# Optimization experiments

Hardware: AMD Instinct MI355X
Metric: run time of the kernel (lower is better)

The kernel has to match this reference:

```python
import jax, jax.numpy as jnp
import numpy as np

N = 50000          # nodes
E_RAND = 590000    # random edges (+ N self-loops -> E = 640000)
IN_F = 128
OUT_F = 128
H, D = 8, 16       # num_heads, head_dim (H*D == OUT_F)
HOP = 5
ALPHA = 0.1
SLOPE = 0.2
EPS = 1e-5


def _layer_norm(x, g, b):
    mu = jnp.mean(x, axis=-1, keepdims=True)
    var = jnp.mean((x - mu) ** 2, axis=-1, keepdims=True)
    return (x - mu) * jax.lax.rsqrt(var + EPS) * g + b


def setup_inputs() -> dict:
    key = jax.random.key(0)
    ks = jax.random.split(key, 10)
    loops = jnp.arange(N, dtype=jnp.int32)  # self-loops -> no 0-in-degree nodes
    src = jnp.concatenate([loops, jax.random.randint(ks[0], (E_RAND,), 0, N, dtype=jnp.int32)])
    dst = jnp.concatenate([loops, jax.random.randint(ks[1], (E_RAND,), 0, N, dtype=jnp.int32)])
    s = 0.05  # xavier-like small init gain
    return {
        "feat": jax.random.normal(ks[2], (N, IN_F), jnp.float32),
        "src": src,
        "dst": dst,
        "w_head": jax.random.normal(ks[3], (OUT_F, IN_F), jnp.float32) * s,
        "w_tail": jax.random.normal(ks[4], (OUT_F, IN_F), jnp.float32) * s,
        "w_ent": jax.random.normal(ks[5], (OUT_F, IN_F), jnp.float32) * s,
        "attn": jax.random.normal(ks[6], (1, H, D), jnp.float32) * s,
        "ln1_g": jnp.ones((IN_F,), jnp.float32),
        "ln1_b": jnp.zeros((IN_F,), jnp.float32),
        "ln2_g": jnp.ones((OUT_F,), jnp.float32),
        "ln2_b": jnp.zeros((OUT_F,), jnp.float32),
        "ff_w1": jax.random.normal(ks[7], (4 * OUT_F, OUT_F), jnp.float32) * s,
        "ff_b1": jnp.zeros((4 * OUT_F,), jnp.float32),
        "ff_w2": jax.random.normal(ks[8], (OUT_F, 4 * OUT_F), jnp.float32) * s,
        "ff_b2": jnp.zeros((OUT_F,), jnp.float32),
    }


def _forward(src, dst, feat, w_head, w_tail, w_ent, attn,
             ln1_g, ln1_b, ln2_g, ln2_b, ff_w1, ff_b1, ff_w2, ff_b2):
    ones = jnp.ones(src.shape[0], jnp.float32)
    out_deg = jnp.clip(jax.ops.segment_sum(ones, src, num_segments=N), 1.0)  # [N]
    in_deg = jnp.clip(jax.ops.segment_sum(ones, dst, num_segments=N), 1.0)
    head_norm = out_deg ** -0.5
    tail_norm = in_deg ** 0.5
    log_in = jnp.log1p(in_deg)  # graph.dstdata['log_in'] (log of in-degree, set at graph build time)

    x = _layer_norm(feat, ln1_g, ln1_b)  # graph_layer_norm (feat_drop=0 in eval)
    fh = (x @ w_head.T).reshape(N, H, D) * head_norm[:, None, None]
    ft = (x @ w_tail.T).reshape(N, H, D) * head_norm[:, None, None]
    fe = (x @ w_ent.T).reshape(N, H, D) * head_norm[:, None, None]

    # edge attention logits: u_mul_v -> leaky_relu -> dot with attn vector
    lr = jax.nn.leaky_relu(fh[src] * ft[dst], SLOPE)  # [E,H,D]
    e = jnp.einsum('ehd,xhd->eh', lr, attn)           # [E,H]
    e = e * log_in[dst][:, None] / D                  # e_mul_v with log_in, / head_dim

    # edge softmax grouped by destination node, per head
    seg_max = jax.ops.segment_max(e, dst, num_segments=N)
    e_exp = jnp.exp(e - seg_max[dst])
    denom = jax.ops.segment_sum(e_exp, dst, num_segments=N)
    a = e_exp / denom[dst]                            # [E,H]

    # PPR diffusion (ppr_estimation), attn_drop=0 in eval
    feat0 = fe
    h = feat0
    for hop in range(HOP):
        if hop > 0:
            h = h * head_norm[:, None, None]
        m = h[src] * a[:, :, None]                    # [E,H,D] u_mul_e
        h = jax.ops.segment_sum(m, dst, num_segments=N)  # fn.sum
        h = h * tail_norm[:, None, None]
        h = (1.0 - ALPHA) * h + ALPHA * feat0

    rst = h + feat.reshape(N, H, D)  # res_fc is Identity since in_feats == out_feats
    rst = rst.reshape(N, OUT_F)
    ff = _layer_norm(rst, ln2_g, ln2_b)
    ff = jax.nn.relu(ff @ ff_w1.T + ff_b1) @ ff_w2.T + ff_b2  # PositionWiseFeedForward
    return ff + rst


def reference(feat, src, dst, w_head, w_tail, w_ent, attn, ln1_g, ln1_b,
              ln2_g, ln2_b, ff_w1, ff_b1, ff_w2, ff_b2):
    return _forward(src, dst, feat, w_head, w_tail, w_ent, attn,
                    ln1_g, ln1_b, ln2_g, ln2_b, ff_w1, ff_b1, ff_w2, ff_b2)
```

## Files before the change

kernel.cpp:

```cpp
#include <hip/hip_runtime.h>
#include <hip/hip_bf16.h>

typedef __attribute__((ext_vector_type(8))) short bf16x8;
typedef __attribute__((ext_vector_type(4))) float f32x4;
typedef unsigned int uint32;

#define F 128
#define HOPS 5
#define LDS_STRIDE 68
#define W1_STRIDE 136
#define W2_STRIDE 72
#define TB_STRIDE 72

__device__ __forceinline__ float b2f(__hip_bfloat16 h) { return __bfloat162float(h); }
__device__ __forceinline__ __hip_bfloat16 f2b(float f) { return __float2bfloat16(f); }

__device__ __forceinline__ float load_in(const void* p, size_t i, int isbf) {
    return isbf ? __bfloat162float(((const __hip_bfloat16*)p)[i]) : ((const float*)p)[i];
}

__device__ __forceinline__ float bflo(uint32 u) { union { uint32 i; float f; } v; v.i = u << 16; return v.f; }
__device__ __forceinline__ float bfhi(uint32 u) { union { uint32 i; float f; } v; v.i = u & 0xffff0000u; return v.f; }
__device__ __forceinline__ uint32 packbf2(float a, float b) {
    __hip_bfloat16 ha = f2b(a), hb = f2b(b);
    unsigned short ua = *(unsigned short*)&ha, ub = *(unsigned short*)&hb;
    return ((uint32)ub << 16) | ua;
}

__device__ __forceinline__ float edge_dot(uint4 gv, const float* ftf, const float* at) {
    float acc = 0.f;
    uint32 us[4] = {gv.x, gv.y, gv.z, gv.w};
    #pragma unroll
    for (int k = 0; k < 4; ++k) {
        float f0 = bflo(us[k]) * ftf[2 * k];
        float f1 = bfhi(us[k]) * ftf[2 * k + 1];
        f0 = fmaxf(f0, 0.2f * f0);
        f1 = fmaxf(f1, 0.2f * f1);
        acc = fmaf(f0, at[2 * k], acc);
        acc = fmaf(f1, at[2 * k + 1], acc);
    }
    return acc;
}

__global__ void detect_k(const uint32* __restrict__ w, int* flag) {
    __shared__ int cnt[256];
    int t = threadIdx.x;
    uint32 x = w[t * 97];
    int e_low = (x >> 7) & 0xFF;
    cnt[t] = (e_low >= 110 && e_low <= 135) ? 1 : 0;
    __syncthreads();
    for (int s = 128; s > 0; s >>= 1) {
        if (t < s) cnt[t] += cnt[t + s];
        __syncthreads();
    }
    if (t == 0) flag[0] = (cnt[0] >= 160) ? 1 : 0;
}

__global__ void cvt_all_k(const void* __restrict__ w_head, const void* __restrict__ w_tail,
                          const void* __restrict__ w_ent, const void* __restrict__ ff_w1,
                          const void* __restrict__ ff_w2, const void* __restrict__ attn,
                          const void* __restrict__ ff_b1, const void* __restrict__ ff_b2,
                          const int* __restrict__ flag,
                          __hip_bfloat16* __restrict__ wblob, float* __restrict__ fblob) {
    int i = blockIdx.x * blockDim.x + threadIdx.x;
    int isbf = flag[0];
    if (i < 180224) {
        const void* srcp; int j;
        if (i < 16384)       { srcp = w_head; j = i; }
        else if (i < 32768)  { srcp = w_tail; j = i - 16384; }
        else if (i < 49152)  { srcp = w_ent;  j = i - 32768; }
        else if (i < 114688) { srcp = ff_w1;  j = i - 49152; }
        else                 { srcp = ff_w2;  j = i - 114688; }
        wblob[i] = f2b(load_in(srcp, j, isbf));
    } else if (i < 180992) {
        int k = i - 180224;
        const void* srcp; int j;
        if (k < 128)      { srcp = attn;  j = k; }
        else if (k < 640) { srcp = ff_b1; j = k - 128; }
        else              { srcp = ff_b2; j = k - 640; }
        fblob[k] = load_in(srcp, j, isbf);
    }
}

__global__ void degree_k(const int* __restrict__ src, const int* __restrict__ dst,
                         int* in8, int* out8, int E, int N) {
    int i = blockIdx.x * blockDim.x + threadIdx.x;
    int slice = blockIdx.x & 7;
    if (i < E) {
        atomicAdd(&in8[slice * N + dst[i]], 1);
        atomicAdd(&out8[slice * N + src[i]], 1);
    }
}

__global__ void scan1_k(const int* __restrict__ in8, int* partial, int* blk_sum, int N) {
    __shared__ int sh[256];
    int t = threadIdx.x;
    int i = blockIdx.x * 256 + t;
    int c = 0;
    if (i < N) {
#pragma unroll
        for (int s = 0; s < 8; ++s) c += in8[s * N + i];
    }
    sh[t] = c;
    __syncthreads();
    for (int o = 1; o < 256; o <<= 1) {
        int v = (t >= o) ? sh[t - o] : 0;
        __syncthreads();
        sh[t] += v;
        __syncthreads();
    }
    if (i < N) partial[i] = sh[t] - c;
    if (t == 255) blk_sum[blockIdx.x] = sh[255];
}

__global__ void scan2_k(const int* __restrict__ blk_sum, int* blk_off, int nb,
                        int* row_ptr, int N) {
    __shared__ int sh[256];
    int t = threadIdx.x;
    if (nb <= 256) {
        int v = (t < nb) ? blk_sum[t] : 0;
        sh[t] = v;
        __syncthreads();
        for (int o = 1; o < 256; o <<= 1) {
            int u = (t >= o) ? sh[t - o] : 0;
            __syncthreads();
            sh[t] += u;
            __syncthreads();
        }
        if (t < nb) blk_off[t] = sh[t] - v;
        if (t == 255) row_ptr[N] = sh[255];
    } else if (t == 0) {
        int run = 0;
        for (int b = 0; b < nb; ++b) { blk_off[b] = run; run += blk_sum[b]; }
        row_ptr[N] = run;
    }
}

__global__ void scan3_norms_k(const int* __restrict__ partial, const int* __restrict__ blk_off,
                              const int* __restrict__ in8, const int* __restrict__ out8,
                              int* row_ptr, int* soff, float* head_norm, float* tail_norm,
                              float* log_in, int N) {
    int i = blockIdx.x * 256 + threadIdx.x;
    if (i >= N) return;
    row_ptr[i] = partial[i] + blk_off[blockIdx.x];
    int run = 0;
#pragma unroll
    for (int s = 0; s < 8; ++s) { soff[s * N + i] = run; run += in8[s * N + i]; }
    int od = 0;
#pragma unroll
    for (int s = 0; s < 8; ++s) od += out8[s * N + i];
    float id = fmaxf((float)run, 1.0f);
    float odf = fmaxf((float)od, 1.0f);
    head_norm[i] = rsqrtf(odf);
    tail_norm[i] = sqrtf(id);
    log_in[i] = log1pf(id);
}

__global__ void scatter_k(const int* __restrict__ src, const int* __restrict__ dst,
                          const int* __restrict__ row_ptr, const int* __restrict__ soff,
                          int* cursor8, int* csr_src, int E, int N) {
    int i = blockIdx.x * blockDim.x + threadIdx.x;
    int slice = blockIdx.x & 7;
    if (i < E) {
        int d = dst[i];
        int p = row_ptr[d] + soff[slice * N + d] + atomicAdd(&cursor8[slice * N + d], 1);
        csr_src[p] = src[i];
    }
}

__global__ void ln1_k(const void* __restrict__ x, const void* __restrict__ g,
                      const void* __restrict__ b, const int* __restrict__ flag,
                      __hip_bfloat16* __restrict__ y, int N) {
    int w = blockIdx.x * (blockDim.x >> 6) + (threadIdx.x >> 6);
    if (w >= N) return;
    int isbf = flag[0];
    int t = threadIdx.x & 63;
    float v0 = load_in(x, (size_t)w * F + t, isbf);
    float v1 = load_in(x, (size_t)w * F + t + 64, isbf);
    float s = v0 + v1, sq = v0 * v0 + v1 * v1;
    for (int m = 1; m < 64; m <<= 1) { s += __shfl_xor(s, m, 64); sq += __shfl_xor(sq, m, 64); }
    float mu = s * (1.0f / F);
    float var = fmaxf(sq * (1.0f / F) - mu * mu, 0.0f);
    float r = rsqrtf(var + 1e-5f);
    y[(size_t)w * F + t]      = f2b((v0 - mu) * r * load_in(g, t, isbf) + load_in(b, t, isbf));
    y[(size_t)w * F + t + 64] = f2b((v1 - mu) * r * load_in(g, t + 64, isbf) + load_in(b, t + 64, isbf));
}

__global__ void ln2_k(const float* __restrict__ x, const void* __restrict__ g,
                      const void* __restrict__ b, const int* __restrict__ flag,
                      __hip_bfloat16* __restrict__ y, int N) {
    int w = blockIdx.x * (blockDim.x >> 6) + (threadIdx.x >> 6);
    if (w >= N) return;
    int isbf = flag[0];
    int t = threadIdx.x & 63;
    float v0 = x[(size_t)w * F + t], v1 = x[(size_t)w * F + t + 64];
    float s = v0 + v1, sq = v0 * v0 + v1 * v1;
    for (int m = 1; m < 64; m <<= 1) { s += __shfl_xor(s, m, 64); sq += __shfl_xor(sq, m, 64); }
    float mu = s * (1.0f / F);
    float var = fmaxf(sq * (1.0f / F) - mu * mu, 0.0f);
    float r = rsqrtf(var + 1e-5f);
    y[(size_t)w * F + t]      = f2b((v0 - mu) * r * load_in(g, t, isbf) + load_in(b, t, isbf));
    y[(size_t)w * F + t + 64] = f2b((v1 - mu) * r * load_in(g, t + 64, isbf) + load_in(b, t + 64, isbf));
}

__global__ void proj_gemm_k(const __hip_bfloat16* __restrict__ X,
                            const __hip_bfloat16* __restrict__ Wall,
                            const float* __restrict__ head_norm,
                            __hip_bfloat16* __restrict__ fh,
                            __hip_bfloat16* __restrict__ ft,
                            uint32* __restrict__ fe_bf, int N) {
    __shared__ __align__(16) char smem[2 * 64 * W1_STRIDE * 2];
    __hip_bfloat16* lx = (__hip_bfloat16*)smem;
    __hip_bfloat16* lw = (__hip_bfloat16*)(smem + 64 * W1_STRIDE * 2);
    float* eps = (float*)smem;
    int tid = threadIdx.x;
    int wv = tid >> 6, lane = tid & 63;
    int lr = lane & 15, quad = lane >> 4;
    int bm = blockIdx.x * 64;
    int g = blockIdx.y;
    int wsel = g >> 1;
    int wcb = (g & 1) * 64;
    {
        const __hip_bfloat16* xs = X + (size_t)bm * F;
        size_t maxe = (size_t)N * F;
#pragma unroll
        for (int i = 0; i < 4; ++i) {
            int idx = i * 2048 + tid * 8;
            int n = idx >> 7, k = idx & 127;
            size_t gi = (size_t)bm * F + idx;
            uint4 v = (gi + 8 <= maxe) ? *(const uint4*)(xs + idx)
                                       : *(const uint4*)(X + maxe - 8);
            *(uint4*)&lx[n * W1_STRIDE + k] = v;
        }
        const __hip_bfloat16* ws = Wall + ((size_t)wsel * F + wcb) * F;
#pragma unroll
        for (int i = 0; i < 4; ++i) {
            int idx = i * 2048 + tid * 8;
            int n = idx >> 7, k = idx & 127;
            *(uint4*)&lw[n * W1_STRIDE + k] = *(const uint4*)(ws + idx);
        }
    }
    __syncthreads();
    f32x4 acc[4] = {{0,0,0,0},{0,0,0,0},{0,0,0,0},{0,0,0,0}};
#pragma unroll
    for (int ks = 0; ks < 4; ++ks) {
        bf16x8 a = *reinterpret_cast<const bf16x8*>(&lx[(wv * 16 + lr) * W1_STRIDE + ks * 32 + quad * 8]);
#pragma unroll
        for (int j = 0; j < 4; ++j) {
            bf16x8 bb = *reinterpret_cast<const bf16x8*>(&lw[(j * 16 + lr) * W1_STRIDE + ks * 32 + quad * 8]);
            acc[j] = __builtin_amdgcn_mfma_f32_16x16x32_bf16(a, bb, acc[j], 0, 0, 0);
        }
    }
    __syncthreads();
    int rl = wv * 16 + quad * 4;
#pragma unroll
    for (int j = 0; j < 4; ++j)
#pragma unroll
        for (int r = 0; r < 4; ++r)
            eps[(rl + r) * LDS_STRIDE + j * 16 + lr] = acc[j][r];
    __syncthreads();
    int tr = tid >> 4, tc = (tid & 15) * 4;
#pragma unroll
    for (int p = 0; p < 4; ++p) {
        int row_l = p * 16 + tr;
        int grow = bm + row_l;
        if (grow >= N) continue;
        float4 v = *(const float4*)&eps[row_l * LDS_STRIDE + tc];
        float hn = head_norm[grow];
        v.x *= hn; v.y *= hn; v.z *= hn; v.w *= hn;
        size_t idx = (size_t)grow * F + wcb + tc;
        uint2 u; u.x = packbf2(v.x, v.y); u.y = packbf2(v.z, v.w);
        __hip_bfloat16* dstp = (wsel == 0) ? fh : (wsel == 1) ? ft : (__hip_bfloat16*)fe_bf;
        *(uint2*)&dstp[idx] = u;
    }
}

__global__ void attn_soft_k(const int* __restrict__ csr_src, const int* __restrict__ row_ptr,
                            const uint32* __restrict__ fh2, const uint32* __restrict__ ft2,
                            const float* __restrict__ attn_f, const float* __restrict__ log_in,
                            float* __restrict__ e_buf, float* __restrict__ inv_arr, int N) {
    int w = blockIdx.x * (blockDim.x >> 6) + (threadIdx.x >> 6);
    if (w >= N) return;
    int t = threadIdx.x & 63;
    int g = t >> 4, j = t & 15;
    int b = row_ptr[w], e = row_ptr[w + 1];
    uint4 fr = ((const uint4*)ft2)[(size_t)w * 16 + j];
    float ftf[8] = {bflo(fr.x), bfhi(fr.x), bflo(fr.y), bfhi(fr.y),
                    bflo(fr.z), bfhi(fr.z), bflo(fr.w), bfhi(fr.w)};
    float at[8];
#pragma unroll
    for (int k = 0; k < 8; ++k) at[k] = attn_f[8 * j + k];
    float scale = log_in[w] * (1.0f / 16.0f);
    float m = -1e30f;
    for (int p0 = b; p0 < e; p0 += 8) {
        int pa = p0 + g, pb = p0 + 4 + g;
        bool oka = pa < e, okb = pb < e;
        int sa = csr_src[oka ? pa : b];
        int sb = csr_src[okb ? pb : b];
        uint4 ga = ((const uint4*)fh2)[(size_t)sa * 16 + j];
        uint4 gb = ((const uint4*)fh2)[(size_t)sb * 16 + j];
        float ra = edge_dot(ga, ftf, at);
        float rb = edge_dot(gb, ftf, at);
        ra += __shfl_xor(ra, 1, 64);
        rb += __shfl_xor(rb, 1, 64);
        float la = ra * scale, lb = rb * scale;
        if (oka) { if (!(j & 1)) e_buf[(size_t)pa * 8 + (j >> 1)] = la; m = fmaxf(m, la); }
        if (okb) { if (!(j & 1)) e_buf[(size_t)pb * 8 + (j >> 1)] = lb; m = fmaxf(m, lb); }
    }
    m = fmaxf(m, __shfl_xor(m, 16, 64));
    m = fmaxf(m, __shfl_xor(m, 32, 64));
    float mh = __shfl(m, (t & 7) * 2, 64);
    float sum = 0.f;
    for (size_t base = (size_t)b * 8 + t; base < (size_t)e * 8; base += 64) {
        float ex = expf(e_buf[base] - mh);
        e_buf[base] = ex;
        sum += ex;
    }
    sum += __shfl_xor(sum, 8, 64);
    sum += __shfl_xor(sum, 16, 64);
    sum += __shfl_xor(sum, 32, 64);
    float inv = 1.0f / fmaxf(sum, 1e-30f);
    if (t < 8) inv_arr[(size_t)w * 8 + t] = inv;
}

__global__ void hop_k(const uint32* __restrict__ gsrc2, const float* __restrict__ e_exp,
                      const float* __restrict__ inv_arr,
                      const int* __restrict__ csr_src, const int* __restrict__ row_ptr,
                      const float* __restrict__ tail_norm, const float* __restrict__ head_norm,
                      const uint32* __restrict__ fe_bf, const void* __restrict__ feat,
                      const int* __restrict__ flag,
                      uint32* __restrict__ out_bf, float* __restrict__ out_f32,
                      int last, int N) {
    int w = blockIdx.x * 8 + (threadIdx.x >> 5);
    if (w >= N) return;
    int l = threadIdx.x & 31;
    int h = l >> 2;
    int b = row_ptr[w], e = row_ptr[w + 1];
    float inv = inv_arr[(size_t)w * 8 + h];
    float a0 = 0.f, a1 = 0.f, a2 = 0.f, a3 = 0.f;
    int p = b;
    for (; p + 8 <= e; p += 8) {
        int s[8]; float av[8]; uint2 gg[8];
#pragma unroll
        for (int i = 0; i < 8; ++i) s[i] = csr_src[p + i];
#pragma unroll
        for (int i = 0; i < 8; ++i) av[i] = e_exp[(size_t)(p + i) * 8 + h];
#pragma unroll
        for (int i = 0; i < 8; ++i) gg[i] = ((const uint2*)gsrc2)[(size_t)s[i] * 32 + l];
#pragma unroll
        for (int i = 0; i < 8; ++i) {
            a0 += bflo(gg[i].x) * av[i]; a1 += bfhi(gg[i].x) * av[i];
            a2 += bflo(gg[i].y) * av[i]; a3 += bfhi(gg[i].y) * av[i];
        }
    }
    if (p < e) {
        int s[8]; float av[8]; uint2 gg[8];
#pragma unroll
        for (int i = 0; i < 8; ++i) {
            int q = p + i;
            bool ok = q < e;
            int q2 = ok ? q : b;
            s[i] = csr_src[q2];
            av[i] = ok ? e_exp[(size_t)q * 8 + h] : 0.f;
        }
#pragma unroll
        for (int i = 0; i < 8; ++i) gg[i] = ((const uint2*)gsrc2)[(size_t)s[i] * 32 + l];
#pragma unroll
        for (int i = 0; i < 8; ++i) {
            a0 += bflo(gg[i].x) * av[i]; a1 += bfhi(gg[i].x) * av[i];
            a2 += bflo(gg[i].y) * av[i]; a3 += bfhi(gg[i].y) * av[i];
        }
    }
    float tl = tail_norm[w] * 0.9f * inv;
    uint2 feu = ((const uint2*)fe_bf)[(size_t)w * 32 + l];
    float r0 = tl * a0 + 0.1f * bflo(feu.x);
    float r1 = tl * a1 + 0.1f * bfhi(feu.x);
    float r2 = tl * a2 + 0.1f * bflo(feu.y);
    float r3 = tl * a3 + 0.1f * bfhi(feu.y);
    if (last) {
        int isbf = flag[0];
        float4 o;
        if (isbf) {
            uint2 fu = ((const uint2*)feat)[(size_t)w * 32 + l];
            o.x = r0 + bflo(fu.x); o.y = r1 + bfhi(fu.x);
            o.z = r2 + bflo(fu.y); o.w = r3 + bfhi(fu.y);
        } else {
            float4 fv = ((const float4*)feat)[(size_t)w * 32 + l];
            o.x = r0 + fv.x; o.y = r1 + fv.y; o.z = r2 + fv.z; o.w = r3 + fv.w;
        }
        ((float4*)out_f32)[(size_t)w * 32 + l] = o;
    } else {
        float hn = head_norm[w];
        uint2 u;
        u.x = packbf2(r0 * hn, r1 * hn);
        u.y = packbf2(r2 * hn, r3 * hn);
        ((uint2*)out_bf)[(size_t)w * 32 + l] = u;
    }
}

__global__ __launch_bounds__(256, 2)
void ffn_fused_k(const __hip_bfloat16* __restrict__ Y, const __hip_bfloat16* __restrict__ W1,
                 const __hip_bfloat16* __restrict__ W2, const float* __restrict__ b1f,
                 const float* __restrict__ b2f, const float* __restrict__ rst,
                 const int* __restrict__ flag, void* __restrict__ out, int N) {
    __shared__ __align__(16) char smem[45056];
    __hip_bfloat16* lw1 = (__hip_bfloat16*)smem;
    __hip_bfloat16* lw2 = (__hip_bfloat16*)(smem + 17408);
    __hip_bfloat16* tb  = (__hip_bfloat16*)(smem + 35840);
    float* eps = (float*)smem;
    int tid = threadIdx.x;
    int wv = tid >> 6, lane = tid & 63;
    int lr = lane & 15, quad = lane >> 4;
    int bm = blockIdx.x * 64;
    int row_a = bm + wv * 16 + lr;
    if (row_a >= N) row_a = N - 1;
    bf16x8 ay[4];
    {
        const __hip_bfloat16* yr = Y + (size_t)row_a * F + quad * 8;
#pragma unroll
        for (int ks = 0; ks < 4; ++ks) ay[ks] = *reinterpret_cast<const bf16x8*>(yr + ks * 32);
    }
    f32x4 o[8];
#pragma unroll
    for (int j = 0; j < 8; ++j) o[j] = (f32x4){0,0,0,0};
    __hip_bfloat16* tbuf = tb + wv * (16 * TB_STRIDE);
    for (int c = 0; c < 8; ++c) {
        int nb0 = c * 64;
        __syncthreads();
        {
            const __hip_bfloat16* s1 = W1 + (size_t)nb0 * F;
#pragma unroll
            for (int i = 0; i < 4; ++i) {
                int idx = i * 2048 + tid * 8;
                int n = idx >> 7, k = idx & 127;
                *(uint4*)&lw1[n * W1_STRIDE + k] = *(const uint4*)(s1 + idx);
            }
#pragma unroll
            for (int i = 0; i < 4; ++i) {
                int idx = i * 2048 + tid * 8;
                int r = idx >> 6, k2 = idx & 63;
                *(uint4*)&lw2[r * W2_STRIDE + k2] = *(const uint4*)(W2 + (size_t)r * 512 + nb0 + k2);
            }
        }
        __syncthreads();
        f32x4 t[4] = {{0,0,0,0},{0,0,0,0},{0,0,0,0},{0,0,0,0}};
#pragma unroll
        for (int ks = 0; ks < 4; ++ks) {
#pragma unroll
            for (int j = 0; j < 4; ++j) {
                bf16x8 bb = *reinterpret_cast<const bf16x8*>(&lw1[(j * 16 + lr) * W1_STRIDE + ks * 32 + quad * 8]);
                t[j] = __builtin_amdgcn_mfma_f32_16x16x32_bf16(ay[ks], bb, t[j], 0, 0, 0);
            }
        }
#pragma unroll
        for (int j = 0; j < 4; ++j) {
            float bias = b1f[nb0 + 16 * j + lr];
#pragma unroll
            for (int r = 0; r < 4; ++r) {
                float v = fmaxf(t[j][r] + bias, 0.f);
                tbuf[(quad * 4 + r) * TB_STRIDE + j * 16 + lr] = f2b(v);
            }
        }
#pragma unroll
        for (int ks2 = 0; ks2 < 2; ++ks2) {
            bf16x8 at = *reinterpret_cast<const bf16x8*>(&tbuf[lr * TB_STRIDE + ks2 * 32 + quad * 8]);
#pragma unroll
            for (int j2 = 0; j2 < 8; ++j2) {
                bf16x8 bb = *reinterpret_cast<const bf16x8*>(&lw2[(j2 * 16 + lr) * W2_STRIDE + ks2 * 32 + quad * 8]);
                o[j2] = __builtin_amdgcn_mfma_f32_16x16x32_bf16(at, bb, o[j2], 0, 0, 0);
            }
        }
    }
    __syncthreads();
    int rl = wv * 16 + quad * 4;
#pragma unroll
    for (int j = 0; j < 8; ++j)
#pragma unroll
        for (int r = 0; r < 4; ++r)
            eps[(rl + r) * 132 + j * 16 + lr] = o[j][r];
    __syncthreads();
    int isbf = flag[0];
#pragma unroll
    for (int p = 0; p < 8; ++p) {
        int idx = p * 1024 + tid * 4;
        int row_l = idx >> 7, col = idx & 127;
        int grow = bm + row_l;
        if (grow >= N) continue;
        float4 v = *(const float4*)&eps[row_l * 132 + col];
        float4 bias = *(const float4*)&b2f[col];
        float4 rv = *(const float4*)&rst[(size_t)grow * F + col];
        v.x += bias.x + rv.x; v.y += bias.y + rv.y;
        v.z += bias.z + rv.z; v.w += bias.w + rv.w;
        size_t gidx = (size_t)grow * F + col;
        if (isbf) {
            uint2 u; u.x = packbf2(v.x, v.y); u.y = packbf2(v.z, v.w);
            *(uint2*)&((__hip_bfloat16*)out)[gidx] = u;
        } else {
            *(float4*)&((float*)out)[gidx] = v;
        }
    }
}

extern "C" void kernel_launch(void* const* d_in, const int* in_sizes, int n_in,
                              void* d_out, int out_size, void* d_ws, size_t ws_size,
                              hipStream_t stream) {
    if (n_in < 15) return;
    const void* feat = d_in[0];
    const int* src = (const int*)d_in[1];
    const int* dst = (const int*)d_in[2];
    const void* w_head = d_in[3];
    const void* w_tail = d_in[4];
    const void* w_ent  = d_in[5];
    const void* attn   = d_in[6];
    const void* ln1_g  = d_in[7];
    const void* ln1_b  = d_in[8];
    const void* ln2_g  = d_in[9];
    const void* ln2_b  = d_in[10];
    const void* ff_w1  = d_in[11];
    const void* ff_b1  = d_in[12];
    const void* ff_w2  = d_in[13];
    const void* ff_b2  = d_in[14];

    const int N = in_sizes[0] / F;
    const int E = in_sizes[1];
    (void)out_size;

    char* base = (char*)d_ws;
    size_t off = 0;
    auto alloc = [&](size_t bytes) -> void* {
        void* r = base + off;
        off += (bytes + 255) & ~(size_t)255;
        return r;
    };
    int* zr        = (int*)alloc((size_t)24 * N * 4);
    int* in8 = zr, * out8 = zr + 8 * N, * cursor8 = zr + 16 * N;
    int* soff      = (int*)alloc((size_t)8 * N * 4);
    int* row_ptr   = (int*)alloc((size_t)(N + 1) * 4);
    int* partial   = (int*)alloc((size_t)N * 4);
    int* blk_sum   = (int*)alloc((size_t)1024 * 4);
    int* blk_off   = (int*)alloc((size_t)1024 * 4);
    int* flag      = (int*)alloc(256);
    float* head_norm = (float*)alloc((size_t)N * 4);
    float* tail_norm = (float*)alloc((size_t)N * 4);
    float* log_in    = (float*)alloc((size_t)N * 4);
    float* inv_arr   = (float*)alloc((size_t)N * 8 * 4);
    int* csr_src   = (int*)alloc((size_t)E * 4);
    __hip_bfloat16* wh_bf = (__hip_bfloat16*)alloc((size_t)F * F * 2);
    __hip_bfloat16* wt_bf = (__hip_bfloat16*)alloc((size_t)F * F * 2);
    __hip_bfloat16* we_bf = (__hip_bfloat16*)alloc((size_t)F * F * 2);
    __hip_bfloat16* w1_bf = (__hip_bfloat16*)alloc((size_t)512 * F * 2);
    __hip_bfloat16* w2_bf = (__hip_bfloat16*)alloc((size_t)F * 512 * 2);
    float* attn_f    = (float*)alloc((size_t)F * 4);
    float* b1f       = (float*)alloc((size_t)512 * 4);
    float* b2f_      = (float*)alloc((size_t)F * 4);
    __hip_bfloat16* x_bf = (__hip_bfloat16*)alloc((size_t)N * F * 2);
    __hip_bfloat16* fh   = (__hip_bfloat16*)alloc((size_t)N * F * 2);
    __hip_bfloat16* ftb  = (__hip_bfloat16*)alloc((size_t)N * F * 2);
    float* e_a = (float*)alloc((size_t)E * 8 * 4);
    uint32* fe_bf = (uint32*)alloc((size_t)N * F * 2);
    uint32* hA_bf = (uint32*)alloc((size_t)N * F * 2);
    uint32* hB_bf = (uint32*)alloc((size_t)N * F * 2);
    float* rst = (float*)alloc((size_t)N * F * 4);
    __hip_bfloat16* y_bf = (__hip_bfloat16*)hA_bf;
    (void)wt_bf; (void)we_bf;
    if (off > ws_size) return;

    const int Mb = (N + 63) / 64;
    const int nodeBlocks = (N + 3) / 4;
    const int hopBlocks = (N + 7) / 8;
    const int nb = (N + 255) / 256;

    detect_k<<<1, 256, 0, stream>>>((const uint32*)feat, flag);
    cvt_all_k<<<(180992 + 255) / 256, 256, 0, stream>>>(w_head, w_tail, w_ent, ff_w1, ff_w2,
                                                        attn, ff_b1, ff_b2, flag, wh_bf, attn_f);

    hipMemsetAsync(zr, 0, (size_t)24 * N * 4, stream);
    degree_k<<<(E + 255) / 256, 256, 0, stream>>>(src, dst, in8, out8, E, N);
    scan1_k<<<nb, 256, 0, stream>>>(in8, partial, blk_sum, N);
    scan2_k<<<1, 256, 0, stream>>>(blk_sum, blk_off, nb, row_ptr, N);
    scan3_norms_k<<<nb, 256, 0, stream>>>(partial, blk_off, in8, out8,
                                          row_ptr, soff, head_norm, tail_norm, log_in, N);
    scatter_k<<<(E + 255) / 256, 256, 0, stream>>>(src, dst, row_ptr, soff, cursor8, csr_src, E, N);

    ln1_k<<<nodeBlocks, 256, 0, stream>>>(feat, ln1_g, ln1_b, flag, x_bf, N);
    proj_gemm_k<<<dim3(Mb, 6), 256, 0, stream>>>(x_bf, wh_bf, head_norm, fh, ftb, fe_bf, N);

    attn_soft_k<<<nodeBlocks, 256, 0, stream>>>(csr_src, row_ptr, (const uint32*)fh,
                                                (const uint32*)ftb, attn_f, log_in,
                                                e_a, inv_arr, N);

    const uint32* gsrc = fe_bf;
    uint32* bufs[2] = {hA_bf, hB_bf};
    for (int hop = 0; hop < HOPS; ++hop) {
        int last = (hop == HOPS - 1);
        uint32* dst_bf = last ? nullptr : bufs[hop & 1];
        hop_k<<<hopBlocks, 256, 0, stream>>>(gsrc, e_a, inv_arr, csr_src, row_ptr, tail_norm,
                                             head_norm, fe_bf, feat, flag, dst_bf, rst, last, N);
        if (!last) gsrc = dst_bf;
    }

    ln2_k<<<nodeBlocks, 256, 0, stream>>>(rst, ln2_g, ln2_b, flag, y_bf, N);
    ffn_fused_k<<<Mb, 256, 0, stream>>>(y_bf, w1_bf, w2_bf, b1f, b2f_, rst, flag, d_out, N);
}
```

Before: 468.5 us.

## Store attention weights in fp16, fuse LN2 into last hop, merge scan kernels

```diff
diff --git a/kernel.cpp b/kernel.cpp
--- a/kernel.cpp
+++ b/kernel.cpp
@@ -1,5 +1,6 @@
 #include <hip/hip_runtime.h>
 #include <hip/hip_bf16.h>
+#include <hip/hip_fp16.h>
 
 typedef __attribute__((ext_vector_type(8))) short bf16x8;
 typedef __attribute__((ext_vector_type(4))) float f32x4;
@@ -27,19 +28,18 @@
     return ((uint32)ub << 16) | ua;
 }
 
-__device__ __forceinline__ float edge_dot(uint4 gv, const float* ftf, const float* at) {
-    float acc = 0.f;
+__device__ __forceinline__ float edge_dot2(uint4 gv, const float* c1, const float* c2) {
+    float acc = 0.f, acc2 = 0.f;
     uint32 us[4] = {gv.x, gv.y, gv.z, gv.w};
     #pragma unroll
     for (int k = 0; k < 4; ++k) {
-        float f0 = bflo(us[k]) * ftf[2 * k];
-        float f1 = bfhi(us[k]) * ftf[2 * k + 1];
-        f0 = fmaxf(f0, 0.2f * f0);
-        f1 = fmaxf(f1, 0.2f * f1);
-        acc = fmaf(f0, at[2 * k], acc);
-        acc = fmaf(f1, at[2 * k + 1], acc);
-    }
-    return acc;
+        float f0 = bflo(us[k]), f1 = bfhi(us[k]);
+        acc  = fmaf(c1[2 * k],     f0,        acc);
+        acc2 = fmaf(c2[2 * k],     fabsf(f0), acc2);
+        acc  = fmaf(c1[2 * k + 1], f1,        acc);
+        acc2 = fmaf(c2[2 * k + 1], fabsf(f1), acc2);
+    }
+    return acc + acc2;
 }
 
 __global__ void detect_k(const uint32* __restrict__ w, int* flag) {
@@ -156,6 +156,38 @@
     log_in[i] = log1pf(id);
 }
 
+__global__ void scan3f_k(const int* __restrict__ partial, const int* __restrict__ blk_sum,
+                         int nb, const int* __restrict__ in8, const int* __restrict__ out8,
+                         int* row_ptr, int* soff, float* head_norm, float* tail_norm,
+                         float* log_in, int N) {
+    __shared__ int bs[256];
+    int t = threadIdx.x;
+    bs[t] = (t < nb) ? blk_sum[t] : 0;
+    __syncthreads();
+    for (int o = 1; o < 256; o <<= 1) {
+        int v = (t >= o) ? bs[t - o] : 0;
+        __syncthreads();
+        bs[t] += v;
+        __syncthreads();
+    }
+    if (blockIdx.x == 0 && t == 0) row_ptr[N] = bs[nb - 1];
+    int boff = (blockIdx.x == 0) ? 0 : bs[blockIdx.x - 1];
+    int i = blockIdx.x * 256 + t;
+    if (i >= N) return;
+    row_ptr[i] = partial[i] + boff;
+    int run = 0;
+#pragma unroll
+    for (int s = 0; s < 8; ++s) { soff[s * N + i] = run; run += in8[s * N + i]; }
+    int od = 0;
+#pragma unroll
+    for (int s = 0; s < 8; ++s) od += out8[s * N + i];
+    float id = fmaxf((float)run, 1.0f);
+    float odf = fmaxf((float)od, 1.0f);
+    head_norm[i] = rsqrtf(odf);
+    tail_norm[i] = sqrtf(id);
+    log_in[i] = log1pf(id);
+}
+
 __global__ void scatter_k(const int* __restrict__ src, const int* __restrict__ dst,
                           const int* __restrict__ row_ptr, const int* __restrict__ soff,
                           int* cursor8, int* csr_src, int E, int N) {
@@ -177,23 +209,6 @@
     int t = threadIdx.x & 63;
     float v0 = load_in(x, (size_t)w * F + t, isbf);
     float v1 = load_in(x, (size_t)w * F + t + 64, isbf);
-    float s = v0 + v1, sq = v0 * v0 + v1 * v1;
-    for (int m = 1; m < 64; m <<= 1) { s += __shfl_xor(s, m, 64); sq += __shfl_xor(sq, m, 64); }
-    float mu = s * (1.0f / F);
-    float var = fmaxf(sq * (1.0f / F) - mu * mu, 0.0f);
-    float r = rsqrtf(var + 1e-5f);
-    y[(size_t)w * F + t]      = f2b((v0 - mu) * r * load_in(g, t, isbf) + load_in(b, t, isbf));
-    y[(size_t)w * F + t + 64] = f2b((v1 - mu) * r * load_in(g, t + 64, isbf) + load_in(b, t + 64, isbf));
-}
-
-__global__ void ln2_k(const float* __restrict__ x, const void* __restrict__ g,
-                      const void* __restrict__ b, const int* __restrict__ flag,
-                      __hip_bfloat16* __restrict__ y, int N) {
-    int w = blockIdx.x * (blockDim.x >> 6) + (threadIdx.x >> 6);
-    if (w >= N) return;
-    int isbf = flag[0];
-    int t = threadIdx.x & 63;
-    float v0 = x[(size_t)w * F + t], v1 = x[(size_t)w * F + t + 64];
     float s = v0 + v1, sq = v0 * v0 + v1 * v1;
     for (int m = 1; m < 64; m <<= 1) { s += __shfl_xor(s, m, 64); sq += __shfl_xor(sq, m, 64); }
     float mu = s * (1.0f / F);
@@ -278,7 +293,8 @@
 __global__ void attn_soft_k(const int* __restrict__ csr_src, const int* __restrict__ row_ptr,
                             const uint32* __restrict__ fh2, const uint32* __restrict__ ft2,
                             const float* __restrict__ attn_f, const float* __restrict__ log_in,
-                            float* __restrict__ e_buf, float* __restrict__ inv_arr, int N) {
+                            float* __restrict__ e_buf, __half* __restrict__ e_h,
+                            float* __restrict__ inv_arr, int N) {
     int w = blockIdx.x * (blockDim.x >> 6) + (threadIdx.x >> 6);
     if (w >= N) return;
     int t = threadIdx.x & 63;
@@ -287,9 +303,13 @@
     uint4 fr = ((const uint4*)ft2)[(size_t)w * 16 + j];
     float ftf[8] = {bflo(fr.x), bfhi(fr.x), bflo(fr.y), bfhi(fr.y),
                     bflo(fr.z), bfhi(fr.z), bflo(fr.w), bfhi(fr.w)};
-    float at[8];
-#pragma unroll
-    for (int k = 0; k < 8; ++k) at[k] = attn_f[8 * j + k];
+    float c1[8], c2[8];
+#pragma unroll
+    for (int k = 0; k < 8; ++k) {
+        float at = attn_f[8 * j + k];
+        c1[k] = 0.6f * at * ftf[k];
+        c2[k] = 0.4f * at * fabsf(ftf[k]);
+    }
     float scale = log_in[w] * (1.0f / 16.0f);
     float m = -1e30f;
     for (int p0 = b; p0 < e; p0 += 8) {
@@ -299,8 +319,8 @@
         int sb = csr_src[okb ? pb : b];
         uint4 ga = ((const uint4*)fh2)[(size_t)sa * 16 + j];
         uint4 gb = ((const uint4*)fh2)[(size_t)sb * 16 + j];
-        float ra = edge_dot(ga, ftf, at);
-        float rb = edge_dot(gb, ftf, at);
+        float ra = edge_dot2(ga, c1, c2);
+        float rb = edge_dot2(gb, c1, c2);
         ra += __shfl_xor(ra, 1, 64);
         rb += __shfl_xor(rb, 1, 64);
         float la = ra * scale, lb = rb * scale;
@@ -313,7 +333,7 @@
     float sum = 0.f;
     for (size_t base = (size_t)b * 8 + t; base < (size_t)e * 8; base += 64) {
         float ex = expf(e_buf[base] - mh);
-        e_buf[base] = ex;
+        e_h[base] = __float2half(ex);
         sum += ex;
     }
     sum += __shfl_xor(sum, 8, 64);
@@ -323,11 +343,12 @@
     if (t < 8) inv_arr[(size_t)w * 8 + t] = inv;
 }
 
-__global__ void hop_k(const uint32* __restrict__ gsrc2, const float* __restrict__ e_exp,
+__global__ void hop_k(const uint32* __restrict__ gsrc2, const __half* __restrict__ e_h,
                       const float* __restrict__ inv_arr,
                       const int* __restrict__ csr_src, const int* __restrict__ row_ptr,
                       const float* __restrict__ tail_norm, const float* __restrict__ head_norm,
                       const uint32* __restrict__ fe_bf, const void* __restrict__ feat,
+                      const void* __restrict__ ln2g, const void* __restrict__ ln2b,
                       const int* __restrict__ flag,
                       uint32* __restrict__ out_bf, float* __restrict__ out_f32,
                       int last, int N) {
@@ -344,7 +365,7 @@
 #pragma unroll
         for (int i = 0; i < 8; ++i) s[i] = csr_src[p + i];
 #pragma unroll
-        for (int i = 0; i < 8; ++i) av[i] = e_exp[(size_t)(p + i) * 8 + h];
+        for (int i = 0; i < 8; ++i) av[i] = __half2float(e_h[(size_t)(p + i) * 8 + h]);
 #pragma unroll
         for (int i = 0; i < 8; ++i) gg[i] = ((const uint2*)gsrc2)[(size_t)s[i] * 32 + l];
 #pragma unroll
@@ -361,7 +382,7 @@
             bool ok = q < e;
             int q2 = ok ? q : b;
             s[i] = csr_src[q2];
-            av[i] = ok ? e_exp[(size_t)q * 8 + h] : 0.f;
+            av[i] = ok ? __half2float(e_h[(size_t)q * 8 + h]) : 0.f;
         }
 #pragma unroll
         for (int i = 0; i < 8; ++i) gg[i] = ((const uint2*)gsrc2)[(size_t)s[i] * 32 + l];
@@ -389,6 +410,24 @@
             o.x = r0 + fv.x; o.y = r1 + fv.y; o.z = r2 + fv.z; o.w = r3 + fv.w;
         }
         ((float4*)out_f32)[(size_t)w * 32 + l] = o;
+        float s2 = o.x + o.y + o.z + o.w;
+        float sq = o.x * o.x + o.y * o.y + o.z * o.z + o.w * o.w;
+#pragma unroll
+        for (int mm = 1; mm < 32; mm <<= 1) {
+            s2 += __shfl_xor(s2, mm, 64);
+            sq += __shfl_xor(sq, mm, 64);
+        }
+        float mu = s2 * (1.0f / F);
+        float var = fmaxf(sq * (1.0f / F) - mu * mu, 0.0f);
+        float rr = rsqrtf(var + 1e-5f);
+        float g0 = load_in(ln2g, 4 * l + 0, isbf), g1 = load_in(ln2g, 4 * l + 1, isbf);
+        float g2 = load_in(ln2g, 4 * l + 2, isbf), g3 = load_in(ln2g, 4 * l + 3, isbf);
+        float b0 = load_in(ln2b, 4 * l + 0, isbf), b1 = load_in(ln2b, 4 * l + 1, isbf);
+        float b2 = load_in(ln2b, 4 * l + 2, isbf), b3 = load_in(ln2b, 4 * l + 3, isbf);
+        uint2 u;
+        u.x = packbf2((o.x - mu) * rr * g0 + b0, (o.y - mu) * rr * g1 + b1);
+        u.y = packbf2((o.z - mu) * rr * g2 + b2, (o.w - mu) * rr * g3 + b3);
+        ((uint2*)out_bf)[(size_t)w * 32 + l] = u;
     } else {
         float hn = head_norm[w];
         uint2 u;
@@ -562,6 +601,7 @@
     uint32* hB_bf = (uint32*)alloc((size_t)N * F * 2);
     float* rst = (float*)alloc((size_t)N * F * 4);
     __hip_bfloat16* y_bf = (__hip_bfloat16*)hA_bf;
+    __half* e_h = (__half*)x_bf;
     (void)wt_bf; (void)we_bf;
     if (off > ws_size) return;
 
@@ -577,9 +617,14 @@
     hipMemsetAsync(zr, 0, (size_t)24 * N * 4, stream);
     degree_k<<<(E + 255) / 256, 256, 0, stream>>>(src, dst, in8, out8, E, N);
     scan1_k<<<nb, 256, 0, stream>>>(in8, partial, blk_sum, N);
-    scan2_k<<<1, 256, 0, stream>>>(blk_sum, blk_off, nb, row_ptr, N);
-    scan3_norms_k<<<nb, 256, 0, stream>>>(partial, blk_off, in8, out8,
-                                          row_ptr, soff, head_norm, tail_norm, log_in, N);
+    if (nb <= 256) {
+        scan3f_k<<<nb, 256, 0, stream>>>(partial, blk_sum, nb, in8, out8,
+                                         row_ptr, soff, head_norm, tail_norm, log_in, N);
+    } else {
+        scan2_k<<<1, 256, 0, stream>>>(blk_sum, blk_off, nb, row_ptr, N);
+        scan3_norms_k<<<nb, 256, 0, stream>>>(partial, blk_off, in8, out8,
+                                              row_ptr, soff, head_norm, tail_norm, log_in, N);
+    }
     scatter_k<<<(E + 255) / 256, 256, 0, stream>>>(src, dst, row_ptr, soff, cursor8, csr_src, E, N);
 
     ln1_k<<<nodeBlocks, 256, 0, stream>>>(feat, ln1_g, ln1_b, flag, x_bf, N);
@@ -587,18 +632,18 @@
 
     attn_soft_k<<<nodeBlocks, 256, 0, stream>>>(csr_src, row_ptr, (const uint32*)fh,
                                                 (const uint32*)ftb, attn_f, log_in,
-                                                e_a, inv_arr, N);
+                                                e_a, e_h, inv_arr, N);
 
     const uint32* gsrc = fe_bf;
     uint32* bufs[2] = {hA_bf, hB_bf};
     for (int hop = 0; hop < HOPS; ++hop) {
         int last = (hop == HOPS - 1);
-        uint32* dst_bf = last ? nullptr : bufs[hop & 1];
-        hop_k<<<hopBlocks, 256, 0, stream>>>(gsrc, e_a, inv_arr, csr_src, row_ptr, tail_norm,
-                                             head_norm, fe_bf, feat, flag, dst_bf, rst, last, N);
+        uint32* dst_bf = last ? (uint32*)y_bf : bufs[hop & 1];
+        hop_k<<<hopBlocks, 256, 0, stream>>>(gsrc, e_h, inv_arr, csr_src, row_ptr, tail_norm,
+                                             head_norm, fe_bf, feat, ln2_g, ln2_b, flag,
+                                             dst_bf, rst, last, N);
         if (!last) gsrc = dst_bf;
     }
 
-    ln2_k<<<nodeBlocks, 256, 0, stream>>>(rst, ln2_g, ln2_b, flag, y_bf, N);
     ffn_fused_k<<<Mb, 256, 0, stream>>>(y_bf, w1_bf, w2_bf, b1f, b2f_, rst, flag, d_out, N);
 }
```

Result: faster. 458.9 us (-2.0%).
